# Kernel optimization log

Hardware: AMD Instinct MI355X
Metric: run time of the kernel (lower is better)

## Reference

```python
import jax, jax.numpy as jnp
import numpy as np

H, DV, DM = 16, 64, 1024   # n_head, d_v, d_model
B, L = 8, 1024             # batch, seq len (len_k == len_v)
LN_EPS = 1e-5


def setup_inputs() -> dict:
    key = jax.random.key(0)
    ks = jax.random.split(key, 8)
    rn = lambda i, shape, scale=1.0: (jax.random.normal(ks[i], shape, jnp.float32) * scale)
    return {
        "q": rn(0, (B, L, DM)),
        "k": rn(1, (B, L, DM)),
        "v": rn(2, (B, L, DM)),
        "posi_att": rn(3, (H, L, L), 0.1),
        "w_k": rn(4, (H, DM), float(np.sqrt(2.0 / (DM + 1)))),
        "b_k": jnp.zeros((H,), jnp.float32),
        "w_v": rn(5, (H * DV, DM), float(np.sqrt(2.0 / (DM + DV)))),
        "b_v": jnp.zeros((H * DV,), jnp.float32),
        "w_fc": rn(6, (DM, H * DV), float(np.sqrt(2.0 / (DM + H * DV)))),
        "b_fc": jnp.zeros((DM,), jnp.float32),
        "ln_g": jnp.ones((DM,), jnp.float32),
        "ln_b": jnp.zeros((DM,), jnp.float32),
    }


def reference(q, k, v, posi_att, w_k, b_k, w_v, b_v, w_fc, b_fc, ln_g, ln_b):
    # q is unused by the original forward (only its device is read)
    b, l, _ = k.shape
    # key projection: d_k == 1, so one scalar per (token, head)
    kk = k @ w_k.T + b_k                               # [b, l, H]
    vv = (v @ w_v.T + b_v).reshape(b, l, H, DV)        # [b, l, H, DV]
    # temperature = sqrt(d_k) = 1.0 -> no-op, kept for faithfulness
    kk = kk / 1.0
    # scores[h, b, i, j] = kk[b, i, h] + posi_att[h, i, j]  (head-major, matches torch view)
    scores = kk.transpose(2, 0, 1)[..., None] + posi_att[:, None, :, :]  # [H, b, l, l]
    diag = jnp.eye(l, dtype=bool)
    scores = jnp.where(diag, -jnp.inf, scores)
    attn = jax.nn.softmax(scores, axis=-1)             # [H, b, l, l]
    # dropout is identity in eval mode
    out = jnp.einsum('hbqk,bkhd->bqhd', attn, vv).reshape(b, l, H * DV)
    out = out @ w_fc.T + b_fc                          # [b, l, DM]
    mu = out.mean(-1, keepdims=True)
    var = out.var(-1, keepdims=True)
    out = (out - mu) / jnp.sqrt(var + LN_EPS) * ln_g + ln_b
    return out, attn.reshape(H * b, l, l)
```

## Files before the change

kernel.cpp:

```cpp
#include <hip/hip_runtime.h>
#include <stdint.h>

#define NH 16
#define NDV 64
#define NDM 1024
#define NB 8
#define NL 1024

typedef __attribute__((ext_vector_type(8))) short short8;
typedef __attribute__((ext_vector_type(4))) short short4v;
typedef __attribute__((ext_vector_type(4))) float f32x4;

static __device__ __forceinline__ unsigned short f2bf(float x) {
    unsigned int u = __builtin_bit_cast(unsigned int, x);
    unsigned int r = (u + 0x7fffu + ((u >> 16) & 1u)) >> 16;
    return (unsigned short)r;
}

static __device__ __forceinline__ float waveMax(float v) {
#pragma unroll
    for (int o = 32; o > 0; o >>= 1) v = fmaxf(v, __shfl_xor(v, o, 64));
    return v;
}
static __device__ __forceinline__ float waveSum(float v) {
#pragma unroll
    for (int o = 32; o > 0; o >>= 1) v += __shfl_xor(v, o, 64);
    return v;
}

static __device__ __forceinline__ void gload_lds16(const void* g, void* l) {
    __builtin_amdgcn_global_load_lds((const __attribute__((address_space(1))) void*)g,
                                     (__attribute__((address_space(3))) void*)l, 16, 0, 0);
}

__global__ __launch_bounds__(256) void phaseA(
    const float* __restrict__ posi, float* __restrict__ attn_out,
    unsigned short* __restrict__ a_bf,
    const float* __restrict__ v, const float* __restrict__ wv, const float* __restrict__ wfc,
    unsigned short* __restrict__ v_bf, unsigned short* __restrict__ wv_bf,
    unsigned short* __restrict__ wfc_bf) {
    __shared__ float red[8];
    const int bid = blockIdx.x;
    const int t = threadIdx.x;
    if (bid < 16384) {
        const int h = bid >> 10, i = bid & 1023;
        const float4* rowp = (const float4*)(posi + (((size_t)h << 10) + i) * 1024);
        float4 p = rowp[t];
        const int j0 = t << 2;
        float* pf = (float*)&p;
        if (i >= j0 && i < j0 + 4) pf[i - j0] = -1e30f;
        float m = fmaxf(fmaxf(pf[0], pf[1]), fmaxf(pf[2], pf[3]));
        m = waveMax(m);
        if ((t & 63) == 0) red[t >> 6] = m;
        __syncthreads();
        m = fmaxf(fmaxf(red[0], red[1]), fmaxf(red[2], red[3]));
        const float e0 = __expf(pf[0] - m), e1 = __expf(pf[1] - m);
        const float e2 = __expf(pf[2] - m), e3 = __expf(pf[3] - m);
        float s = waveSum(e0 + e1 + e2 + e3);
        if ((t & 63) == 0) red[4 + (t >> 6)] = s;
        __syncthreads();
        s = red[4] + red[5] + red[6] + red[7];
        const float inv = 1.0f / s;
        float4 a;
        a.x = e0 * inv; a.y = e1 * inv; a.z = e2 * inv; a.w = e3 * inv;
        float* base = attn_out + (((size_t)(h << 3)) << 20) + ((size_t)i << 10);
#pragma unroll
        for (int b = 0; b < 8; ++b)
            ((float4*)(base + ((size_t)b << 20)))[t] = a;
        short4v u;
        u[0] = (short)f2bf(a.x); u[1] = (short)f2bf(a.y);
        u[2] = (short)f2bf(a.z); u[3] = (short)f2bf(a.w);
        *(short4v*)(a_bf + ((((size_t)h << 10) + i) << 10) + j0) = u;
    } else {
        int b = bid - 16384;
        const float* src;
        unsigned short* dst;
        if (b < 8192)      { src = v;   dst = v_bf; }
        else if (b < 9216) { src = wv;  dst = wv_bf;  b -= 8192; }
        else               { src = wfc; dst = wfc_bf; b -= 9216; }
        const size_t idx = ((size_t)b * 256 + t) << 2;
        const float4 x = *(const float4*)(src + idx);
        short4v u;
        u[0] = (short)f2bf(x.x); u[1] = (short)f2bf(x.y);
        u[2] = (short)f2bf(x.z); u[3] = (short)f2bf(x.w);
        *(short4v*)(dst + idx) = u;
    }
}

template <int EPI>
static __device__ __forceinline__ void gemm128_core(
    const unsigned short* __restrict__ A,
    const unsigned short* __restrict__ Bt,
    const float* __restrict__ bias,
    void* __restrict__ Cout,
    const int K, const int tm, const int tn, const int bh,
    unsigned short* sA, unsigned short* sB) {
    const int tid = threadIdx.x;
    const int lane = tid & 63;
    const int w = tid >> 6;
    const int wr = w >> 1, wc = w & 1;

    const unsigned short* Ab = A + (size_t)tm * 128 * K;
    const unsigned short* Bb = Bt + (size_t)tn * 128 * K;

    const int r0 = w * 32 + (lane >> 2);
    const int ch = lane & 3;
    const int so = ((ch ^ ((r0 >> 1) & 3)) << 3);
    const unsigned short* gA0 = Ab + (size_t)r0 * K + so;
    const unsigned short* gA1 = Ab + (size_t)(r0 + 16) * K + so;
    const unsigned short* gB0 = Bb + (size_t)r0 * K + so;
    const unsigned short* gB1 = Bb + (size_t)(r0 + 16) * K + so;
    const int ldsOff = w * 1024;

    const int c = lane >> 4;
    int offA[4], offB[4];
#pragma unroll
    for (int f = 0; f < 4; ++f) {
        const int fra = wr * 64 + f * 16 + (lane & 15);
        offA[f] = fra * 32 + ((c ^ ((fra >> 1) & 3)) << 3);
        const int frb = wc * 64 + f * 16 + (lane & 15);
        offB[f] = frb * 32 + ((c ^ ((frb >> 1) & 3)) << 3);
    }

    f32x4 acc[4][4];
#pragma unroll
    for (int i = 0; i < 4; ++i)
#pragma unroll
        for (int j = 0; j < 4; ++j) acc[i][j] = (f32x4){0.f, 0.f, 0.f, 0.f};

    const int nst = K >> 5;

#pragma unroll
    for (int p = 0; p < 2; ++p) {
        unsigned short* lA = sA + (p << 12) + ldsOff;
        unsigned short* lB = sB + (p << 12) + ldsOff;
        const int kt = p << 5;
        gload_lds16(gA0 + kt, lA);
        gload_lds16(gA1 + kt, lA + 512);
        gload_lds16(gB0 + kt, lB);
        gload_lds16(gB1 + kt, lB + 512);
    }

    int cur = 0;
    for (int t = 0; t < nst; ++t) {
        if (t + 1 < nst) {
            asm volatile("s_waitcnt vmcnt(4)" ::: "memory");
        } else {
            asm volatile("s_waitcnt vmcnt(0)" ::: "memory");
        }
        __builtin_amdgcn_s_barrier();
        __builtin_amdgcn_sched_barrier(0);
        if (t + 2 < nst) {
            const int sb = (cur + 2 >= 3) ? cur - 1 : cur + 2;
            unsigned short* lA = sA + (sb << 12) + ldsOff;
            unsigned short* lB = sB + (sb << 12) + ldsOff;
            const int kt = (t + 2) << 5;
            gload_lds16(gA0 + kt, lA);
            gload_lds16(gA1 + kt, lA + 512);
            gload_lds16(gB0 + kt, lB);
            gload_lds16(gB1 + kt, lB + 512);
        }
        const unsigned short* bA = sA + (cur << 12);
        const unsigned short* bB = sB + (cur << 12);
        short8 af[4], bfv[4];
#pragma unroll
        for (int f = 0; f < 4; ++f) af[f] = *(const short8*)&bA[offA[f]];
#pragma unroll
        for (int f = 0; f < 4; ++f) bfv[f] = *(const short8*)&bB[offB[f]];
        __builtin_amdgcn_s_setprio(1);
#pragma unroll
        for (int i = 0; i < 4; ++i)
#pragma unroll
            for (int j = 0; j < 4; ++j)
                acc[i][j] = __builtin_amdgcn_mfma_f32_16x16x32_bf16(af[i], bfv[j], acc[i][j], 0, 0, 0);
        __builtin_amdgcn_s_setprio(0);
        cur = (cur == 2) ? 0 : cur + 1;
    }

#pragma unroll
    for (int i = 0; i < 4; ++i) {
        const int gRow0 = tm * 128 + wr * 64 + i * 16 + ((lane >> 4) << 2);
#pragma unroll
        for (int j = 0; j < 4; ++j) {
            const int gCol = tn * 128 + wc * 64 + j * 16 + (lane & 15);
            f32x4 v = acc[i][j];
            if (EPI == 1) {
                const float bb2 = bias[gCol];
                const int hh = gCol >> 6, dd = gCol & 63;
                const int b = gRow0 >> 10, ll2 = gRow0 & 1023;
                unsigned short* C = (unsigned short*)Cout;
                short4v u;
                u[0] = (short)f2bf(v[0] + bb2);
                u[1] = (short)f2bf(v[1] + bb2);
                u[2] = (short)f2bf(v[2] + bb2);
                u[3] = (short)f2bf(v[3] + bb2);
                *(short4v*)(C + (size_t)hh * 524288 + ((size_t)b * 64 + dd) * 1024 + ll2) = u;
            } else if (EPI == 2) {
                const int b = gCol >> 6, dd = gCol & 63;
                unsigned short* X = (unsigned short*)Cout;
#pragma unroll
                for (int r = 0; r < 4; ++r)
                    X[((size_t)b * 1024 + gRow0 + r) * 1024 + bh * 64 + dd] = f2bf(v[r]);
            } else {
                const float bb2 = bias[gCol];
                float* O = (float*)Cout;
#pragma unroll
                for (int r = 0; r < 4; ++r)
                    O[(size_t)(gRow0 + r) * 1024 + gCol] = v[r] + bb2;
            }
        }
    }
}

__global__ __launch_bounds__(256) void gemm_k1(const unsigned short* __restrict__ A,
                                               const unsigned short* __restrict__ Bt,
                                               const float* __restrict__ bias,
                                               unsigned short* __restrict__ C) {
    __shared__ unsigned short sA[12288], sB[12288];
    const int s = (blockIdx.x & 7) * 64 + (blockIdx.x >> 3);
    gemm128_core<1>(A, Bt, bias, C, 1024, s >> 3, s & 7, 0, sA, sB);
}

__global__ __launch_bounds__(256) void gemm_k2(const unsigned short* __restrict__ A,
                                               const unsigned short* __restrict__ Bt,
                                               unsigned short* __restrict__ X) {
    __shared__ unsigned short sA[12288], sB[12288];
    const int s = (blockIdx.x & 7) * 64 + (blockIdx.x >> 3);
    const int bh = s >> 5;
    gemm128_core<2>(A + (size_t)bh * 1048576, Bt + (size_t)bh * 524288, nullptr, X,
                    1024, (s >> 2) & 7, s & 3, bh, sA, sB);
}

__global__ __launch_bounds__(256) void gemm_k3(const unsigned short* __restrict__ A,
                                               const unsigned short* __restrict__ Bt,
                                               const float* __restrict__ bias,
                                               float* __restrict__ O) {
    __shared__ unsigned short sA[12288], sB[12288];
    const int s = (blockIdx.x & 7) * 64 + (blockIdx.x >> 3);
    gemm128_core<3>(A, Bt, bias, O, 1024, s >> 3, s & 7, 0, sA, sB);
}

__global__ __launch_bounds__(256) void ln_kernel(float* __restrict__ out,
                                                 const float* __restrict__ g,
                                                 const float* __restrict__ b) {
    __shared__ float red[8];
    const int row = blockIdx.x, t = threadIdx.x;
    float4* p = (float4*)(out + ((size_t)row << 10));
    float4 x = p[t];
    float s = x.x + x.y + x.z + x.w;
    float sq = x.x * x.x + x.y * x.y + x.z * x.z + x.w * x.w;
    s = waveSum(s);
    sq = waveSum(sq);
    if ((t & 63) == 0) { red[t >> 6] = s; red[4 + (t >> 6)] = sq; }
    __syncthreads();
    s = red[0] + red[1] + red[2] + red[3];
    sq = red[4] + red[5] + red[6] + red[7];
    const float mu = s * (1.f / 1024.f);
    const float var = sq * (1.f / 1024.f) - mu * mu;
    const float rinv = rsqrtf(var + 1e-5f);
    const float4 gg = ((const float4*)g)[t];
    const float4 bb = ((const float4*)b)[t];
    x.x = (x.x - mu) * rinv * gg.x + bb.x;
    x.y = (x.y - mu) * rinv * gg.y + bb.y;
    x.z = (x.z - mu) * rinv * gg.z + bb.z;
    x.w = (x.w - mu) * rinv * gg.w + bb.w;
    p[t] = x;
}

extern "C" void kernel_launch(void* const* d_in, const int* in_sizes, int n_in,
                              void* d_out, int out_size, void* d_ws, size_t ws_size,
                              hipStream_t stream) {
    const float* v    = (const float*)d_in[2];
    const float* posi = (const float*)d_in[3];
    const float* w_v  = (const float*)d_in[6];
    const float* b_v  = (const float*)d_in[7];
    const float* w_fc = (const float*)d_in[8];
    const float* b_fc = (const float*)d_in[9];
    const float* ln_g = (const float*)d_in[10];
    const float* ln_b = (const float*)d_in[11];

    float* out = (float*)d_out;
    float* attn_out = out + (size_t)NB * NL * NDM;

    char* ws = (char*)d_ws;
    unsigned short* A_bf   = (unsigned short*)(ws);
    unsigned short* v_bf   = (unsigned short*)(ws + 33554432);
    unsigned short* wv_bf  = (unsigned short*)(ws + 50331648);
    unsigned short* wfc_bf = (unsigned short*)(ws + 52428800);
    unsigned short* vvT    = (unsigned short*)(ws + 54525952);
    unsigned short* X      = (unsigned short*)(ws + 71303168);

    phaseA<<<26624, 256, 0, stream>>>(posi, attn_out, A_bf, v, w_v, w_fc, v_bf, wv_bf, wfc_bf);
    gemm_k1<<<512, 256, 0, stream>>>(v_bf, wv_bf, b_v, vvT);
    gemm_k2<<<512, 256, 0, stream>>>(A_bf, vvT, X);
    gemm_k3<<<512, 256, 0, stream>>>(X, wfc_bf, b_fc, out);
    ln_kernel<<<8192, 256, 0, stream>>>(out, ln_g, ln_b);
}
```

Measured before the change: 248.5 us.

## Enlarge GEMM tiles to 256x128 with 512-thread blocks and XCD-aware mapping

The three GEMMs now use 256x128 output tiles computed by 8 waves per 512-thread block, where before they used 128x128 tiles with 4 waves. Each wave still owns a 64x64 sub-tile, and the B tile loads are shared across more rows, cutting global traffic per FLOP. The batched attention GEMM also maps blocks so each XCD handles whole heads, which should improve L2 locality. In exchange there are half as many blocks (256 on 256 CUs) and LDS use per block doubles, so occupancy and load balance may suffer.

```diff
diff --git a/kernel.cpp b/kernel.cpp
--- a/kernel.cpp
+++ b/kernel.cpp
@@ -88,7 +88,7 @@
 }
 
 template <int EPI>
-static __device__ __forceinline__ void gemm128_core(
+static __device__ __forceinline__ void gemm256x128_core(
     const unsigned short* __restrict__ A,
     const unsigned short* __restrict__ Bt,
     const float* __restrict__ bias,
@@ -98,19 +98,23 @@
     const int tid = threadIdx.x;
     const int lane = tid & 63;
     const int w = tid >> 6;
-    const int wr = w >> 1, wc = w & 1;
-
-    const unsigned short* Ab = A + (size_t)tm * 128 * K;
+    const int wr = w >> 1;
+    const int wc = w & 1;
+
+    const unsigned short* Ab = A + (size_t)tm * 256 * K;
     const unsigned short* Bb = Bt + (size_t)tn * 128 * K;
 
-    const int r0 = w * 32 + (lane >> 2);
+    const int lr = lane >> 2;
     const int ch = lane & 3;
-    const int so = ((ch ^ ((r0 >> 1) & 3)) << 3);
-    const unsigned short* gA0 = Ab + (size_t)r0 * K + so;
-    const unsigned short* gA1 = Ab + (size_t)(r0 + 16) * K + so;
-    const unsigned short* gB0 = Bb + (size_t)r0 * K + so;
-    const unsigned short* gB1 = Bb + (size_t)(r0 + 16) * K + so;
-    const int ldsOff = w * 1024;
+    const int ra0 = w * 32 + lr;
+    const int rb0 = w * 16 + lr;
+    const int soA = ((ch ^ ((ra0 >> 1) & 3)) << 3);
+    const int soB = ((ch ^ ((rb0 >> 1) & 3)) << 3);
+    const unsigned short* gA0 = Ab + (size_t)ra0 * K + soA;
+    const unsigned short* gA1 = Ab + (size_t)(ra0 + 16) * K + soA;
+    const unsigned short* gB0 = Bb + (size_t)rb0 * K + soB;
+    const int ldsA = w * 1024;
+    const int ldsB = w * 512;
 
     const int c = lane >> 4;
     int offA[4], offB[4];
@@ -130,37 +134,33 @@
 
     const int nst = K >> 5;
 
-#pragma unroll
-    for (int p = 0; p < 2; ++p) {
-        unsigned short* lA = sA + (p << 12) + ldsOff;
-        unsigned short* lB = sB + (p << 12) + ldsOff;
-        const int kt = p << 5;
-        gload_lds16(gA0 + kt, lA);
-        gload_lds16(gA1 + kt, lA + 512);
-        gload_lds16(gB0 + kt, lB);
-        gload_lds16(gB1 + kt, lB + 512);
-    }
+#define STAGE_STEP(sbuf, kt)                                  \
+    {                                                         \
+        unsigned short* lA = sA + ((sbuf) << 13) + ldsA;      \
+        unsigned short* lB = sB + ((sbuf) << 12) + ldsB;      \
+        gload_lds16(gA0 + (kt), lA);                          \
+        gload_lds16(gA1 + (kt), lA + 512);                    \
+        gload_lds16(gB0 + (kt), lB);                          \
+    }
+
+    STAGE_STEP(0, 0)
+    STAGE_STEP(1, 32)
 
     int cur = 0;
     for (int t = 0; t < nst; ++t) {
         if (t + 1 < nst) {
-            asm volatile("s_waitcnt vmcnt(4)" ::: "memory");
+            asm volatile("s_waitcnt vmcnt(3)" ::: "memory");
         } else {
             asm volatile("s_waitcnt vmcnt(0)" ::: "memory");
         }
         __builtin_amdgcn_s_barrier();
         __builtin_amdgcn_sched_barrier(0);
         if (t + 2 < nst) {
-            const int sb = (cur + 2 >= 3) ? cur - 1 : cur + 2;
-            unsigned short* lA = sA + (sb << 12) + ldsOff;
-            unsigned short* lB = sB + (sb << 12) + ldsOff;
+            int sb = cur + 2; if (sb >= 3) sb -= 3;
             const int kt = (t + 2) << 5;
-            gload_lds16(gA0 + kt, lA);
-            gload_lds16(gA1 + kt, lA + 512);
-            gload_lds16(gB0 + kt, lB);
-            gload_lds16(gB1 + kt, lB + 512);
+            STAGE_STEP(sb, kt)
         }
-        const unsigned short* bA = sA + (cur << 12);
+        const unsigned short* bA = sA + (cur << 13);
         const unsigned short* bB = sB + (cur << 12);
         short8 af[4], bfv[4];
 #pragma unroll
@@ -176,10 +176,11 @@
         __builtin_amdgcn_s_setprio(0);
         cur = (cur == 2) ? 0 : cur + 1;
     }
+#undef STAGE_STEP
 
 #pragma unroll
     for (int i = 0; i < 4; ++i) {
-        const int gRow0 = tm * 128 + wr * 64 + i * 16 + ((lane >> 4) << 2);
+        const int gRow0 = tm * 256 + wr * 64 + i * 16 + ((lane >> 4) << 2);
 #pragma unroll
         for (int j = 0; j < 4; ++j) {
             const int gCol = tn * 128 + wc * 64 + j * 16 + (lane & 15);
@@ -212,32 +213,32 @@
     }
 }
 
-__global__ __launch_bounds__(256) void gemm_k1(const unsigned short* __restrict__ A,
+__global__ __launch_bounds__(512) void gemm_k1(const unsigned short* __restrict__ A,
                                                const unsigned short* __restrict__ Bt,
                                                const float* __restrict__ bias,
                                                unsigned short* __restrict__ C) {
-    __shared__ unsigned short sA[12288], sB[12288];
-    const int s = (blockIdx.x & 7) * 64 + (blockIdx.x >> 3);
-    gemm128_core<1>(A, Bt, bias, C, 1024, s >> 3, s & 7, 0, sA, sB);
-}
-
-__global__ __launch_bounds__(256) void gemm_k2(const unsigned short* __restrict__ A,
+    __shared__ unsigned short sA[24576], sB[12288];
+    gemm256x128_core<1>(A, Bt, bias, C, 1024, blockIdx.x >> 3, blockIdx.x & 7, 0, sA, sB);
+}
+
+__global__ __launch_bounds__(512) void gemm_k2(const unsigned short* __restrict__ A,
                                                const unsigned short* __restrict__ Bt,
                                                unsigned short* __restrict__ X) {
-    __shared__ unsigned short sA[12288], sB[12288];
-    const int s = (blockIdx.x & 7) * 64 + (blockIdx.x >> 3);
-    const int bh = s >> 5;
-    gemm128_core<2>(A + (size_t)bh * 1048576, Bt + (size_t)bh * 524288, nullptr, X,
-                    1024, (s >> 2) & 7, s & 3, bh, sA, sB);
-}
-
-__global__ __launch_bounds__(256) void gemm_k3(const unsigned short* __restrict__ A,
+    __shared__ unsigned short sA[24576], sB[12288];
+    const int xcd = blockIdx.x & 7;
+    const int q = blockIdx.x >> 3;
+    const int bh = xcd * 2 + (q >> 4);
+    const int r = q & 15;
+    gemm256x128_core<2>(A + (size_t)bh * 1048576, Bt + (size_t)bh * 524288, nullptr, X,
+                        1024, r >> 2, r & 3, bh, sA, sB);
+}
+
+__global__ __launch_bounds__(512) void gemm_k3(const unsigned short* __restrict__ A,
                                                const unsigned short* __restrict__ Bt,
                                                const float* __restrict__ bias,
                                                float* __restrict__ O) {
-    __shared__ unsigned short sA[12288], sB[12288];
-    const int s = (blockIdx.x & 7) * 64 + (blockIdx.x >> 3);
-    gemm128_core<3>(A, Bt, bias, O, 1024, s >> 3, s & 7, 0, sA, sB);
+    __shared__ unsigned short sA[24576], sB[12288];
+    gemm256x128_core<3>(A, Bt, bias, O, 1024, blockIdx.x >> 3, blockIdx.x & 7, 0, sA, sB);
 }
 
 __global__ __launch_bounds__(256) void ln_kernel(float* __restrict__ out,
@@ -291,8 +292,8 @@
     unsigned short* X      = (unsigned short*)(ws + 71303168);
 
     phaseA<<<26624, 256, 0, stream>>>(posi, attn_out, A_bf, v, w_v, w_fc, v_bf, wv_bf, wfc_bf);
-    gemm_k1<<<512, 256, 0, stream>>>(v_bf, wv_bf, b_v, vvT);
-    gemm_k2<<<512, 256, 0, stream>>>(A_bf, vvT, X);
-    gemm_k3<<<512, 256, 0, stream>>>(X, wfc_bf, b_fc, out);
+    gemm_k1<<<256, 512, 0, stream>>>(v_bf, wv_bf, b_v, vvT);
+    gemm_k2<<<256, 512, 0, stream>>>(A_bf, vvT, X);
+    gemm_k3<<<256, 512, 0, stream>>>(X, wfc_bf, b_fc, out);
     ln_kernel<<<8192, 256, 0, stream>>>(out, ln_g, ln_b);
 }
```

Result: slower. 259.1 us (+4.3%).

## Restructure GEMM pipeline to 64-wide K double buffer and nontemporal attn stores

Applied to the files above, without the earlier changes.

The shared GEMM core now stages 64-element K slices into two LDS buffers, where it previously used three buffers of 32-element slices. It uses an 8-way XOR swizzle and runs two MFMA sub-steps per barrier pair, which halves the number of loop iterations and barriers. The fp32 attention output, written eight times per row, now uses nontemporal stores so it does not pollute the cache. The GEMM change raises LDS use per block and shrinks prefetch depth from two stages to one, which may expose more global-load latency or lower occupancy.

```diff
diff --git a/kernel.cpp b/kernel.cpp
--- a/kernel.cpp
+++ b/kernel.cpp
@@ -61,15 +61,15 @@
         __syncthreads();
         s = red[4] + red[5] + red[6] + red[7];
         const float inv = 1.0f / s;
-        float4 a;
-        a.x = e0 * inv; a.y = e1 * inv; a.z = e2 * inv; a.w = e3 * inv;
+        f32x4 a;
+        a[0] = e0 * inv; a[1] = e1 * inv; a[2] = e2 * inv; a[3] = e3 * inv;
         float* base = attn_out + (((size_t)(h << 3)) << 20) + ((size_t)i << 10);
 #pragma unroll
         for (int b = 0; b < 8; ++b)
-            ((float4*)(base + ((size_t)b << 20)))[t] = a;
+            __builtin_nontemporal_store(a, (f32x4*)(base + ((size_t)b << 20)) + t);
         short4v u;
-        u[0] = (short)f2bf(a.x); u[1] = (short)f2bf(a.y);
-        u[2] = (short)f2bf(a.z); u[3] = (short)f2bf(a.w);
+        u[0] = (short)f2bf(a[0]); u[1] = (short)f2bf(a[1]);
+        u[2] = (short)f2bf(a[2]); u[3] = (short)f2bf(a[3]);
         *(short4v*)(a_bf + ((((size_t)h << 10) + i) << 10) + j0) = u;
     } else {
         int b = bid - 16384;
@@ -103,24 +103,19 @@
     const unsigned short* Ab = A + (size_t)tm * 128 * K;
     const unsigned short* Bb = Bt + (size_t)tn * 128 * K;
 
-    const int r0 = w * 32 + (lane >> 2);
-    const int ch = lane & 3;
-    const int so = ((ch ^ ((r0 >> 1) & 3)) << 3);
-    const unsigned short* gA0 = Ab + (size_t)r0 * K + so;
-    const unsigned short* gA1 = Ab + (size_t)(r0 + 16) * K + so;
-    const unsigned short* gB0 = Bb + (size_t)r0 * K + so;
-    const unsigned short* gB1 = Bb + (size_t)(r0 + 16) * K + so;
-    const int ldsOff = w * 1024;
-
-    const int c = lane >> 4;
-    int offA[4], offB[4];
-#pragma unroll
-    for (int f = 0; f < 4; ++f) {
-        const int fra = wr * 64 + f * 16 + (lane & 15);
-        offA[f] = fra * 32 + ((c ^ ((fra >> 1) & 3)) << 3);
-        const int frb = wc * 64 + f * 16 + (lane & 15);
-        offB[f] = frb * 32 + ((c ^ ((frb >> 1) & 3)) << 3);
-    }
+    const int lrow = lane >> 3;
+    const int lch = lane & 7;
+
+    int offA[2][4], offB[2][4];
+#pragma unroll
+    for (int ks = 0; ks < 2; ++ks)
+#pragma unroll
+        for (int f = 0; f < 4; ++f) {
+            const int fra = wr * 64 + f * 16 + (lane & 15);
+            offA[ks][f] = fra * 64 + ((ks * 4 + (lane >> 4)) ^ (fra & 7)) * 8;
+            const int frb = wc * 64 + f * 16 + (lane & 15);
+            offB[ks][f] = frb * 64 + ((ks * 4 + (lane >> 4)) ^ (frb & 7)) * 8;
+        }
 
     f32x4 acc[4][4];
 #pragma unroll
@@ -128,54 +123,53 @@
 #pragma unroll
         for (int j = 0; j < 4; ++j) acc[i][j] = (f32x4){0.f, 0.f, 0.f, 0.f};
 
-    const int nst = K >> 5;
-
-#pragma unroll
-    for (int p = 0; p < 2; ++p) {
-        unsigned short* lA = sA + (p << 12) + ldsOff;
-        unsigned short* lB = sB + (p << 12) + ldsOff;
-        const int kt = p << 5;
-        gload_lds16(gA0 + kt, lA);
-        gload_lds16(gA1 + kt, lA + 512);
-        gload_lds16(gB0 + kt, lB);
-        gload_lds16(gB1 + kt, lB + 512);
-    }
-
-    int cur = 0;
+    const int nst = K >> 6;
+
+#define STAGE64(buf, kt)                                                          \
+    {                                                                             \
+        unsigned short* dA = sA + ((buf) << 13);                                  \
+        unsigned short* dB = sB + ((buf) << 13);                                  \
+        _Pragma("unroll")                                                         \
+        for (int g = 0; g < 4; ++g) {                                             \
+            const int row = w * 32 + g * 8 + lrow;                                \
+            const int sc = ((lch ^ (row & 7)) << 3);                              \
+            gload_lds16(Ab + (size_t)row * K + (kt) + sc, dA + (w * 32 + g * 8) * 64); \
+            gload_lds16(Bb + (size_t)row * K + (kt) + sc, dB + (w * 32 + g * 8) * 64); \
+        }                                                                         \
+    }
+
+    STAGE64(0, 0)
+
     for (int t = 0; t < nst; ++t) {
+        __builtin_amdgcn_s_barrier();
+        __builtin_amdgcn_sched_barrier(0);
         if (t + 1 < nst) {
-            asm volatile("s_waitcnt vmcnt(4)" ::: "memory");
+            STAGE64((t + 1) & 1, (t + 1) << 6)
+            asm volatile("s_waitcnt vmcnt(8)" ::: "memory");
         } else {
             asm volatile("s_waitcnt vmcnt(0)" ::: "memory");
         }
         __builtin_amdgcn_s_barrier();
         __builtin_amdgcn_sched_barrier(0);
-        if (t + 2 < nst) {
-            const int sb = (cur + 2 >= 3) ? cur - 1 : cur + 2;
-            unsigned short* lA = sA + (sb << 12) + ldsOff;
-            unsigned short* lB = sB + (sb << 12) + ldsOff;
-            const int kt = (t + 2) << 5;
-            gload_lds16(gA0 + kt, lA);
-            gload_lds16(gA1 + kt, lA + 512);
-            gload_lds16(gB0 + kt, lB);
-            gload_lds16(gB1 + kt, lB + 512);
-        }
-        const unsigned short* bA = sA + (cur << 12);
-        const unsigned short* bB = sB + (cur << 12);
-        short8 af[4], bfv[4];
-#pragma unroll
-        for (int f = 0; f < 4; ++f) af[f] = *(const short8*)&bA[offA[f]];
-#pragma unroll
-        for (int f = 0; f < 4; ++f) bfv[f] = *(const short8*)&bB[offB[f]];
-        __builtin_amdgcn_s_setprio(1);
-#pragma unroll
-        for (int i = 0; i < 4; ++i)
-#pragma unroll
-            for (int j = 0; j < 4; ++j)
-                acc[i][j] = __builtin_amdgcn_mfma_f32_16x16x32_bf16(af[i], bfv[j], acc[i][j], 0, 0, 0);
-        __builtin_amdgcn_s_setprio(0);
-        cur = (cur == 2) ? 0 : cur + 1;
-    }
+        const unsigned short* bA = sA + ((t & 1) << 13);
+        const unsigned short* bB = sB + ((t & 1) << 13);
+#pragma unroll
+        for (int ks = 0; ks < 2; ++ks) {
+            short8 af[4], bfv[4];
+#pragma unroll
+            for (int f = 0; f < 4; ++f) af[f] = *(const short8*)&bA[offA[ks][f]];
+#pragma unroll
+            for (int f = 0; f < 4; ++f) bfv[f] = *(const short8*)&bB[offB[ks][f]];
+            __builtin_amdgcn_s_setprio(1);
+#pragma unroll
+            for (int i = 0; i < 4; ++i)
+#pragma unroll
+                for (int j = 0; j < 4; ++j)
+                    acc[i][j] = __builtin_amdgcn_mfma_f32_16x16x32_bf16(af[i], bfv[j], acc[i][j], 0, 0, 0);
+            __builtin_amdgcn_s_setprio(0);
+        }
+    }
+#undef STAGE64
 
 #pragma unroll
     for (int i = 0; i < 4; ++i) {
@@ -216,7 +210,7 @@
                                                const unsigned short* __restrict__ Bt,
                                                const float* __restrict__ bias,
                                                unsigned short* __restrict__ C) {
-    __shared__ unsigned short sA[12288], sB[12288];
+    __shared__ unsigned short sA[16384], sB[16384];
     const int s = (blockIdx.x & 7) * 64 + (blockIdx.x >> 3);
     gemm128_core<1>(A, Bt, bias, C, 1024, s >> 3, s & 7, 0, sA, sB);
 }
@@ -224,7 +218,7 @@
 __global__ __launch_bounds__(256) void gemm_k2(const unsigned short* __restrict__ A,
                                                const unsigned short* __restrict__ Bt,
                                                unsigned short* __restrict__ X) {
-    __shared__ unsigned short sA[12288], sB[12288];
+    __shared__ unsigned short sA[16384], sB[16384];
     const int s = (blockIdx.x & 7) * 64 + (blockIdx.x >> 3);
     const int bh = s >> 5;
     gemm128_core<2>(A + (size_t)bh * 1048576, Bt + (size_t)bh * 524288, nullptr, X,
@@ -235,7 +229,7 @@
                                                const unsigned short* __restrict__ Bt,
                                                const float* __restrict__ bias,
                                                float* __restrict__ O) {
-    __shared__ unsigned short sA[12288], sB[12288];
+    __shared__ unsigned short sA[16384], sB[16384];
     const int s = (blockIdx.x & 7) * 64 + (blockIdx.x >> 3);
     gemm128_core<3>(A, Bt, bias, O, 1024, s >> 3, s & 7, 0, sA, sB);
 }
```

New measurement: 215.6 us. 13.3% less time.
